# Performance work log

Measured on AMD Instinct MI355X. Metric: run time of the kernel, lower is better.

## Reference

```python
import jax, jax.numpy as jnp
import numpy as np

N = 100000       # nodes
E = 1600000      # edges per graph
D_IN, D_H, D_OUT = 256, 64, 32
TEM = (0.9, 0.8)  # tem[0], tem[1]


def setup_inputs() -> dict:
    key = jax.random.key(0)
    ks = jax.random.split(key, 17)
    f32 = jnp.float32
    return {
        "features": jax.random.normal(ks[0], (N, D_IN), f32),
        # GraphConv layer1: glorot-ish weight [in, out] + bias
        "W1": jax.random.normal(ks[1], (D_IN, D_H), f32) / np.sqrt(D_IN).astype(np.float32),
        "b1": jnp.zeros((D_H,), f32),
        "W2": jax.random.normal(ks[2], (D_H, D_OUT), f32) / np.sqrt(D_H).astype(np.float32),
        "b2": jnp.zeros((D_OUT,), f32),
        # gating linears: nn.Linear(2*d, 1) -> weight [1, 2*d], bias [1]
        "ga11_w": jax.random.normal(ks[3], (1, 2 * D_H), f32) * 0.1,
        "ga11_b": jnp.zeros((1,), f32),
        "ga12_w": jax.random.normal(ks[4], (1, 2 * D_H), f32) * 0.1,
        "ga12_b": jnp.zeros((1,), f32),
        "ga21_w": jax.random.normal(ks[5], (1, 2 * D_OUT), f32) * 0.1,
        "ga21_b": jnp.zeros((1,), f32),
        "ga22_w": jax.random.normal(ks[6], (1, 2 * D_OUT), f32) * 0.1,
        "ga22_b": jnp.zeros((1,), f32),
        # two graphs as edge lists over the same N nodes
        "src1": jax.random.randint(ks[7], (E,), 0, N, jnp.int32),
        "dst1": jax.random.randint(ks[8], (E,), 0, N, jnp.int32),
        "src2": jax.random.randint(ks[9], (E,), 0, N, jnp.int32),
        "dst2": jax.random.randint(ks[10], (E,), 0, N, jnp.int32),
    }


def _graph_conv(feat, W, b, src, dst):
    """DGL GraphConv, norm='both': D_dst^{-1/2} A^T D_src^{-1/2} X W + b.
    in_feats > out_feats for both layers, so W is applied before aggregation."""
    ones = jnp.ones(src.shape[0], feat.dtype)
    deg_out = jnp.clip(jax.ops.segment_sum(ones, src, num_segments=N), 1.0)  # [N]
    deg_in = jnp.clip(jax.ops.segment_sum(ones, dst, num_segments=N), 1.0)   # [N]
    h = (feat * jax.lax.rsqrt(deg_out)[:, None]) @ W                          # [N, d_out]
    agg = jax.ops.segment_sum(h[src], dst, num_segments=N)                    # SpMM scatter-add
    return agg * jax.lax.rsqrt(deg_in)[:, None] + b


def _gate(xa, xb, w, b, tem):
    """Faithful to: ga = softmax(Linear(cat[xa,xb]), dim=1); diag(ga) -> ga[0,0];
    xb' = tem * diag * xb. softmax over a size-1 axis gives ones; dropout is a
    no-op in eval mode."""
    ga = jnp.concatenate([xa, xb], axis=1) @ w.T + b  # [N, 1]
    ga = jax.nn.softmax(ga, axis=1)                   # all ones ([N,1], axis of size 1)
    d = ga[0, 0]                                      # torch.diag of [N,1] -> scalar ga[0,0]
    return tem * d * xb


def reference(features, W1, b1, W2, b2, ga11_w, ga11_b, ga12_w, ga12_b,
              ga21_w, ga21_b, ga22_w, ga22_b, src1, dst1, src2, dst2):
    x11 = _graph_conv(features, W1, b1, src1, dst1)
    x12 = _graph_conv(features, W1, b1, src2, dst2)
    x12 = _gate(x11, x12, ga11_w, ga11_b, TEM[1])
    x11 = _gate(x12, x11, ga12_w, ga12_b, TEM[0])
    x1 = x11 + x12
    x21 = _graph_conv(x1, W2, b2, src1, dst1)
    x22 = _graph_conv(x1, W2, b2, src2, dst2)
    x22 = _gate(x21, x22, ga21_w, ga21_b, TEM[1])
    x21 = _gate(x22, x21, ga22_w, ga22_b, TEM[0])
    return x21 + x22
```

## Files before the change

kernel.cpp:

```cpp
#include <hip/hip_runtime.h>
#include <hip/hip_bf16.h>

#define TEM0 0.9f
#define TEM1 0.8f
#define NPB 256
#define CAP 4608
#define CHUNKE 2048
#define MAXBUCK 512

typedef __attribute__((ext_vector_type(8))) short bf16x8;
typedef __attribute__((ext_vector_type(4))) float f32x4;

static __device__ __forceinline__ short f2bf(float x) {
  union { __hip_bfloat16 h; short s; } u;
  u.h = __float2bfloat16(x);
  return u.s;
}
static __device__ __forceinline__ float bf2f(short s) {
  union { float f; unsigned u; } v;
  v.u = ((unsigned)(unsigned short)s) << 16;
  return v.f;
}

__global__ __launch_bounds__(256) void bucket_gemm(
    const int* __restrict__ src1, const int* __restrict__ dst1,
    const int* __restrict__ src2, const int* __restrict__ dst2,
    int* gcur_d, int* gcur_s,
    int* __restrict__ rawD1, int* __restrict__ rawD2,
    unsigned char* __restrict__ rawS1, unsigned char* __restrict__ rawS2,
    int E, int NCH, int NBUCK,
    const float* __restrict__ X, const short* __restrict__ Wb,
    short* __restrict__ Yb, int n)
{
  __shared__ int outR[CHUNKE];
  __shared__ unsigned char outS[CHUNKE];
  __shared__ unsigned short tickD[CHUNKE];
  __shared__ unsigned short tickS[CHUNKE];
  __shared__ short bktD[CHUNKE];
  __shared__ short bktS[CHUNKE];
  __shared__ int histD[MAXBUCK], histS[MAXBUCK];
  __shared__ int strtD[MAXBUCK], strtS[MAXBUCK];
  __shared__ int baszD[MAXBUCK], baszS[MAXBUCK];
  __shared__ int wsumD[4], wsumS[4];

  const int nbB = 2 * NCH;
  const int nbG = (n + 63) / 64;
  const int half = nbB < nbG ? nbB : nbG;
  int bi = (int)blockIdx.x;
  bool isB;
  int bid;
  if (bi < 2 * half) { isB = ((bi & 1) == 0); bid = bi >> 1; }
  else               { isB = (nbB > nbG);     bid = bi - half; }

  if (isB) {
    int g = 0, cb = bid;
    if (cb >= NCH) { g = 1; cb -= NCH; }
    const int* src = g ? src2 : src1;
    const int* dst = g ? dst2 : dst1;
    int* rawD = g ? rawD2 : rawD1;
    unsigned char* rawS = g ? rawS2 : rawS1;
    int* curD = gcur_d + g * NBUCK;
    int* curS = gcur_s + g * NBUCK;
    int tid = threadIdx.x;
    int lane = tid & 63, wave = tid >> 6;
    int e0 = cb * CHUNKE;
    int K = min(CHUNKE, E - e0);

    histD[tid] = 0; histD[tid + 256] = 0;
    histS[tid] = 0; histS[tid + 256] = 0;
    __syncthreads();

    for (int i = tid; i < K; i += 256) {
      int d = dst[e0 + i], s = src[e0 + i];
      tickD[i] = (unsigned short)atomicAdd(&histD[d >> 8], 1);
      tickS[i] = (unsigned short)atomicAdd(&histS[s >> 8], 1);
    }
    __syncthreads();

    {
      int d0 = histD[2 * tid], d1 = histD[2 * tid + 1];
      int s0 = histS[2 * tid], s1 = histS[2 * tid + 1];
      int dv = d0 + d1, sv = s0 + s1;
      int vd = dv, vs = sv;
#pragma unroll
      for (int off = 1; off < 64; off <<= 1) {
        int td = __shfl_up(vd, off);
        int ts = __shfl_up(vs, off);
        if (lane >= off) { vd += td; vs += ts; }
      }
      if (lane == 63) { wsumD[wave] = vd; wsumS[wave] = vs; }
      __syncthreads();
      int wpD = 0, wpS = 0;
#pragma unroll
      for (int w0 = 0; w0 < 4; ++w0) {
        wpD += (w0 < wave) ? wsumD[w0] : 0;
        wpS += (w0 < wave) ? wsumS[w0] : 0;
      }
      int exD = wpD + vd - dv;
      int exS = wpS + vs - sv;
      strtD[2 * tid] = exD; strtD[2 * tid + 1] = exD + d0;
      strtS[2 * tid] = exS; strtS[2 * tid + 1] = exS + s0;
      for (int b = tid; b < NBUCK; b += 256) {
        int c = histD[b];
        baszD[b] = c ? atomicAdd(&curD[b], c) : 0;
        c = histS[b];
        baszS[b] = c ? atomicAdd(&curS[b], c) : 0;
      }
    }
    __syncthreads();

    for (int i = tid; i < K; i += 256) {
      int d = dst[e0 + i], s = src[e0 + i];
      int bD = d >> 8, bS = s >> 8;
      int qD = strtD[bD] + (int)tickD[i];
      int qS = strtS[bS] + (int)tickS[i];
      outR[qD] = ((d & 255) << 17) | s;
      bktD[qD] = (short)bD;
      outS[qS] = (unsigned char)(s & 255);
      bktS[qS] = (short)bS;
    }
    __syncthreads();

    for (int i = tid; i < K; i += 256) {
      int b = bktD[i];
      int off = baszD[b] + (i - strtD[b]);
      if (off < CAP) rawD[(size_t)b * CAP + off] = outR[i];
    }
    for (int i = tid; i < K; i += 256) {
      int b = bktS[i];
      int off = baszS[b] + (i - strtS[b]);
      if (off < CAP) rawS[(size_t)b * CAP + off] = outS[i];
    }
  } else {
    int w = threadIdx.x >> 6;
    int l = threadIdx.x & 63;
    int row = bid * 64 + w * 16 + (l & 15);
    int rowc = row < n ? row : n - 1;
    int ko = (l >> 4) << 3;

    f32x4 acc[4] = {};
    const float* xrow = X + (size_t)rowc * 256;

#pragma unroll
    for (int kk = 0; kk < 8; ++kk) {
      const float4* p = reinterpret_cast<const float4*>(xrow + kk * 32 + ko);
      float4 a0 = p[0], a1 = p[1];
      bf16x8 af;
      af[0] = f2bf(a0.x); af[1] = f2bf(a0.y); af[2] = f2bf(a0.z); af[3] = f2bf(a0.w);
      af[4] = f2bf(a1.x); af[5] = f2bf(a1.y); af[6] = f2bf(a1.z); af[7] = f2bf(a1.w);
#pragma unroll
      for (int ct = 0; ct < 4; ++ct) {
        bf16x8 bfrag = *reinterpret_cast<const bf16x8*>(Wb + ((size_t)(ct * 8 + kk) * 64 + l) * 8);
        acc[ct] = __builtin_amdgcn_mfma_f32_16x16x32_bf16(af, bfrag, acc[ct], 0, 0, 0);
      }
    }

    int r0 = bid * 64 + w * 16 + ((l >> 4) << 2);
    int c0 = l & 15;
#pragma unroll
    for (int ct = 0; ct < 4; ++ct) {
#pragma unroll
      for (int i = 0; i < 4; ++i) {
        int r = r0 + i;
        if (r < n) Yb[(size_t)r * 64 + ct * 16 + c0] = f2bf(acc[ct][i]);
      }
    }
  }
}

__global__ __launch_bounds__(256) void histsort(
    const int* __restrict__ gcur_s, const int* __restrict__ gcur_d,
    const unsigned char* __restrict__ rawS1, const unsigned char* __restrict__ rawS2,
    const int* __restrict__ rawD1, const int* __restrict__ rawD2,
    int* __restrict__ co1, int* __restrict__ co2,
    int* __restrict__ edata1, int* __restrict__ edata2,
    int* __restrict__ ci1, int* __restrict__ ci2,
    int* __restrict__ ns1, int* __restrict__ ns2, int NBUCK, int N)
{
  __shared__ int hist[NPB], strt[NPB];
  __shared__ short tick[CAP];
  __shared__ int sl[CAP];
  __shared__ int wsum[4];

  int bi = (int)blockIdx.x;
  bool isHist = ((bi & 1) == 0);
  int bid = bi >> 1;
  int g = 0, b = bid;
  if (b >= NBUCK) { g = 1; b -= NBUCK; }
  int tid = threadIdx.x;

  if (isHist) {
    const unsigned char* raw = (g ? rawS2 : rawS1) + (size_t)b * CAP;
    int* co = g ? co2 : co1;
    int K = gcur_s[g * NBUCK + b]; if (K > CAP) K = CAP;
    hist[tid] = 0;
    __syncthreads();
    for (int j = tid; j < K; j += 256) atomicAdd(&hist[raw[j]], 1);
    __syncthreads();
    int node = b * NPB + tid;
    if (node < N) co[node] = hist[tid];
  } else {
    const int* raw = (g ? rawD2 : rawD1) + (size_t)b * CAP;
    int* edata = g ? edata2 : edata1;
    int* ci = g ? ci2 : ci1;
    int* ns = g ? ns2 : ns1;
    int K = gcur_d[g * NBUCK + b]; if (K > CAP) K = CAP;
    int lane = tid & 63, wave = tid >> 6;

    hist[tid] = 0;
    __syncthreads();
    for (int j = tid; j < K; j += 256)
      tick[j] = (short)atomicAdd(&hist[raw[j] >> 17], 1);
    __syncthreads();
    int h = hist[tid], v = h;
#pragma unroll
    for (int off = 1; off < 64; off <<= 1) {
      int t = __shfl_up(v, off);
      if (lane >= off) v += t;
    }
    if (lane == 63) wsum[wave] = v;
    __syncthreads();
    int wpre = 0;
#pragma unroll
    for (int w0 = 0; w0 < 4; ++w0) wpre += (w0 < wave) ? wsum[w0] : 0;
    strt[tid] = wpre + v - h;
    __syncthreads();
    for (int j = tid; j < K; j += 256) {
      int r = raw[j];
      sl[strt[r >> 17] + tick[j]] = r & 0x1FFFF;
    }
    __syncthreads();
    size_t gbase = (size_t)b * CAP;
    for (int j = tid; j < K; j += 256) edata[gbase + j] = sl[j];
    int node = b * NPB + tid;
    if (node < N) { ci[node] = hist[tid]; ns[node] = (int)gbase + strt[tid]; }
  }
}

__global__ __launch_bounds__(256) void prep_w(
    const float* __restrict__ W1, const float* __restrict__ W2,
    short* __restrict__ Wb, short* __restrict__ Wb2)
{
  int t = blockIdx.x * 256 + threadIdx.x;
  if (t < 2048) {
    int lane = t & 63;
    int kk = (t >> 6) & 7;
    int ct = t >> 9;
    int col = ct * 16 + (lane & 15);
    int k0 = kk * 32 + ((lane >> 4) << 3);
#pragma unroll
    for (int i = 0; i < 8; ++i)
      Wb[(size_t)t * 8 + i] = f2bf(W1[(size_t)(k0 + i) * 64 + col]);
  } else if (t < 3072) {
    int t2 = t - 2048;
    int lane = t2 & 63;
    int kk = (t2 >> 6) & 1;
    int ct = t2 >> 7;
    int col = ct * 16 + (lane & 15);
    int k0 = kk * 32 + ((lane >> 4) << 3);
#pragma unroll
    for (int i = 0; i < 8; ++i)
      Wb2[(size_t)t2 * 8 + i] = f2bf(W2[(size_t)(k0 + i) * 32 + col]);
  }
}

__global__ __launch_bounds__(256) void gemm2_mfma(
    const short* __restrict__ X, const short* __restrict__ Wb2,
    short* __restrict__ Y2b, int n)
{
  int w = threadIdx.x >> 6;
  int l = threadIdx.x & 63;
  int row = blockIdx.x * 64 + w * 16 + (l & 15);
  int rowc = row < n ? row : n - 1;
  int ko = (l >> 4) << 3;

  f32x4 acc[2] = {};
  const short* xrow = X + (size_t)rowc * 64;

#pragma unroll
  for (int kk = 0; kk < 2; ++kk) {
    bf16x8 af = *reinterpret_cast<const bf16x8*>(xrow + kk * 32 + ko);
#pragma unroll
    for (int ct = 0; ct < 2; ++ct) {
      bf16x8 bfrag = *reinterpret_cast<const bf16x8*>(Wb2 + ((size_t)(ct * 2 + kk) * 64 + l) * 8);
      acc[ct] = __builtin_amdgcn_mfma_f32_16x16x32_bf16(af, bfrag, acc[ct], 0, 0, 0);
    }
  }

  int r0 = blockIdx.x * 64 + w * 16 + ((l >> 4) << 2);
  int c0 = l & 15;
#pragma unroll
  for (int ct = 0; ct < 2; ++ct) {
#pragma unroll
    for (int i = 0; i < 4; ++i) {
      int r = r0 + i;
      if (r < n) Y2b[(size_t)r * 32 + ct * 16 + c0] = f2bf(acc[ct][i]);
    }
  }
}

template<int D, bool BF16OUT>
__global__ __launch_bounds__(256) void gather_nodes_bf(
    const int* __restrict__ ci1, const int* __restrict__ ns1,
    const int* __restrict__ edata1, const int* __restrict__ co1,
    const int* __restrict__ ci2, const int* __restrict__ ns2,
    const int* __restrict__ edata2, const int* __restrict__ co2,
    const short* __restrict__ Yb, const float* __restrict__ bias,
    float bscale, float* __restrict__ outf, short* __restrict__ outb, int n)
{
  constexpr int LPR = D / 8;
  constexpr int EPI = 64 / LPR;
  int wid  = (blockIdx.x * 256 + threadIdx.x) >> 6;
  int lane = threadIdx.x & 63;
  int grp = lane / LPR;
  int li  = lane % LPR;
  if (wid >= n) return;

  const bf16x8* Y8 = reinterpret_cast<const bf16x8*>(Yb);
  float a1[8], a2[8];
#pragma unroll
  for (int k = 0; k < 8; ++k) { a1[k] = 0.f; a2[k] = 0.f; }

  int len1 = ci1[wid], st1 = ns1[wid];
  int len2 = ci2[wid], st2 = ns2[wid];
  int lmax = len1 > len2 ? len1 : len2;

#pragma unroll 2
  for (int j = grp; j < lmax; j += EPI) {
    bool p1 = j < len1, p2 = j < len2;
    int s1 = p1 ? edata1[st1 + j] : 0;
    int s2 = p2 ? edata2[st2 + j] : 0;
    float c1 = p1 ? TEM0 * rsqrtf((float)co1[s1]) : 0.f;
    float c2 = p2 ? TEM1 * rsqrtf((float)co2[s2]) : 0.f;
    bf16x8 v1 = Y8[(size_t)s1 * LPR + li];
    bf16x8 v2 = Y8[(size_t)s2 * LPR + li];
#pragma unroll
    for (int k = 0; k < 8; ++k) {
      a1[k] = fmaf(c1, bf2f(v1[k]), a1[k]);
      a2[k] = fmaf(c2, bf2f(v2[k]), a2[k]);
    }
  }

  float r1 = rsqrtf((float)(len1 < 1 ? 1 : len1));
  float r2 = rsqrtf((float)(len2 < 1 ? 1 : len2));
  float acc[8];
#pragma unroll
  for (int k = 0; k < 8; ++k) acc[k] = fmaf(r1, a1[k], r2 * a2[k]);

#pragma unroll
  for (int m = LPR; m < 64; m <<= 1) {
#pragma unroll
    for (int k = 0; k < 8; ++k) acc[k] += __shfl_xor(acc[k], m);
  }

  if (grp == 0) {
    float4 b0 = reinterpret_cast<const float4*>(bias)[li * 2];
    float4 b1v = reinterpret_cast<const float4*>(bias)[li * 2 + 1];
    float o[8];
    o[0] = fmaf(bscale, b0.x, acc[0]);
    o[1] = fmaf(bscale, b0.y, acc[1]);
    o[2] = fmaf(bscale, b0.z, acc[2]);
    o[3] = fmaf(bscale, b0.w, acc[3]);
    o[4] = fmaf(bscale, b1v.x, acc[4]);
    o[5] = fmaf(bscale, b1v.y, acc[5]);
    o[6] = fmaf(bscale, b1v.z, acc[6]);
    o[7] = fmaf(bscale, b1v.w, acc[7]);
    if constexpr (BF16OUT) {
      bf16x8 ov;
#pragma unroll
      for (int k = 0; k < 8; ++k) ov[k] = f2bf(o[k]);
      *reinterpret_cast<bf16x8*>(outb + (size_t)wid * D + li * 8) = ov;
    } else {
      float4 o0 = make_float4(o[0], o[1], o[2], o[3]);
      float4 o1 = make_float4(o[4], o[5], o[6], o[7]);
      float4* op = reinterpret_cast<float4*>(outf + (size_t)wid * D + li * 8);
      op[0] = o0;
      op[1] = o1;
    }
  }
}

extern "C" void kernel_launch(void* const* d_in, const int* in_sizes, int n_in,
                              void* d_out, int out_size, void* d_ws, size_t ws_size,
                              hipStream_t stream)
{
  const float* features = (const float*)d_in[0];
  const float* W1 = (const float*)d_in[1];
  const float* b1 = (const float*)d_in[2];
  const float* W2 = (const float*)d_in[3];
  const float* b2 = (const float*)d_in[4];
  const int* src1 = (const int*)d_in[13];
  const int* dst1 = (const int*)d_in[14];
  const int* src2 = (const int*)d_in[15];
  const int* dst2 = (const int*)d_in[16];

  const int N = in_sizes[0] / 256;
  const int E = in_sizes[13];
  const int NBUCK = (N + NPB - 1) / NPB;
  const int NCH = (E + CHUNKE - 1) / CHUNKE;

  char* ws = (char*)d_ws;
  int* gcur_d = (int*)ws;
  int* gcur_s = gcur_d + 2 * NBUCK;
  int* rawD1  = gcur_s + 2 * NBUCK;
  int* rawD2  = rawD1 + (size_t)NBUCK * CAP;
  unsigned char* rawS1 = (unsigned char*)(rawD2 + (size_t)NBUCK * CAP);
  unsigned char* rawS2 = rawS1 + (size_t)NBUCK * CAP;
  int* edata1 = (int*)(rawS2 + (size_t)NBUCK * CAP);
  int* edata2 = edata1 + (size_t)NBUCK * CAP;
  int* ci1 = edata2 + (size_t)NBUCK * CAP;
  int* ci2 = ci1 + N;
  int* ns1 = ci2 + N;
  int* ns2 = ns1 + N;
  int* co1 = ns2 + N;
  int* co2 = co1 + N;
  short* Yb  = (short*)(co2 + N);
  short* Y2b = Yb + (size_t)N * 64;
  short* x1b = Y2b + (size_t)N * 32;
  short* Wb  = x1b + (size_t)N * 64;
  short* Wb2 = Wb + 16384;
  float* out = (float*)d_out;

  (void)hipMemsetAsync(gcur_d, 0, (size_t)4 * NBUCK * sizeof(int), stream);
  prep_w<<<12, 256, 0, stream>>>(W1, W2, Wb, Wb2);

  const int nbGemm = (N + 63) / 64;
  bucket_gemm<<<2 * NCH + nbGemm, 256, 0, stream>>>(
      src1, dst1, src2, dst2, gcur_d, gcur_s,
      rawD1, rawD2, rawS1, rawS2, E, NCH, NBUCK,
      features, Wb, Yb, N);

  histsort<<<4 * NBUCK, 256, 0, stream>>>(
      gcur_s, gcur_d, rawS1, rawS2, rawD1, rawD2,
      co1, co2, edata1, edata2, ci1, ci2, ns1, ns2, NBUCK, N);

  gather_nodes_bf<64, true><<<(N + 3) / 4, 256, 0, stream>>>(
      ci1, ns1, edata1, co1, ci2, ns2, edata2, co2,
      Yb, b1, TEM0 + TEM1, nullptr, x1b, N);

  gemm2_mfma<<<nbGemm, 256, 0, stream>>>(x1b, Wb2, Y2b, N);

  gather_nodes_bf<32, false><<<(N + 3) / 4, 256, 0, stream>>>(
      ci1, ns1, edata1, co1, ci2, ns2, edata2, co2,
      Y2b, b2, TEM0 + TEM1, out, nullptr, N);
}
```

Before: 317.4 us.

## Pack per-edge source norm coefficient into edge index word, split histsort kernel

```diff
diff --git a/kernel.cpp b/kernel.cpp
--- a/kernel.cpp
+++ b/kernel.cpp
@@ -168,12 +168,31 @@
   }
 }
 
-__global__ __launch_bounds__(256) void histsort(
-    const int* __restrict__ gcur_s, const int* __restrict__ gcur_d,
+__global__ __launch_bounds__(256) void hist_src(
+    const int* __restrict__ gcur_s,
     const unsigned char* __restrict__ rawS1, const unsigned char* __restrict__ rawS2,
+    int* __restrict__ co1, int* __restrict__ co2, int NBUCK, int N)
+{
+  __shared__ int hist[NPB];
+  int g = 0, b = blockIdx.x;
+  if (b >= NBUCK) { g = 1; b -= NBUCK; }
+  const unsigned char* raw = (g ? rawS2 : rawS1) + (size_t)b * CAP;
+  int* co = g ? co2 : co1;
+  int K = gcur_s[g * NBUCK + b]; if (K > CAP) K = CAP;
+  int tid = threadIdx.x;
+  hist[tid] = 0;
+  __syncthreads();
+  for (int j = tid; j < K; j += 256) atomicAdd(&hist[raw[j]], 1);
+  __syncthreads();
+  int node = b * NPB + tid;
+  if (node < N) co[node] = hist[tid];
+}
+
+__global__ __launch_bounds__(256) void sort_dst(
+    const int* __restrict__ gcur_d,
     const int* __restrict__ rawD1, const int* __restrict__ rawD2,
-    int* __restrict__ co1, int* __restrict__ co2,
-    int* __restrict__ edata1, int* __restrict__ edata2,
+    unsigned* __restrict__ edata1, unsigned* __restrict__ edata2,
+    const int* __restrict__ co1, const int* __restrict__ co2,
     int* __restrict__ ci1, int* __restrict__ ci2,
     int* __restrict__ ns1, int* __restrict__ ns2, int NBUCK, int N)
 {
@@ -181,60 +200,50 @@
   __shared__ short tick[CAP];
   __shared__ int sl[CAP];
   __shared__ int wsum[4];
-
-  int bi = (int)blockIdx.x;
-  bool isHist = ((bi & 1) == 0);
-  int bid = bi >> 1;
-  int g = 0, b = bid;
+  int g = 0, b = blockIdx.x;
   if (b >= NBUCK) { g = 1; b -= NBUCK; }
+  const int* raw = (g ? rawD2 : rawD1) + (size_t)b * CAP;
+  unsigned* edata = g ? edata2 : edata1;
+  const int* co = g ? co2 : co1;
+  const float tem = g ? TEM1 : TEM0;
+  int* ci = g ? ci2 : ci1;
+  int* ns = g ? ns2 : ns1;
+  int K = gcur_d[g * NBUCK + b]; if (K > CAP) K = CAP;
   int tid = threadIdx.x;
-
-  if (isHist) {
-    const unsigned char* raw = (g ? rawS2 : rawS1) + (size_t)b * CAP;
-    int* co = g ? co2 : co1;
-    int K = gcur_s[g * NBUCK + b]; if (K > CAP) K = CAP;
-    hist[tid] = 0;
-    __syncthreads();
-    for (int j = tid; j < K; j += 256) atomicAdd(&hist[raw[j]], 1);
-    __syncthreads();
-    int node = b * NPB + tid;
-    if (node < N) co[node] = hist[tid];
-  } else {
-    const int* raw = (g ? rawD2 : rawD1) + (size_t)b * CAP;
-    int* edata = g ? edata2 : edata1;
-    int* ci = g ? ci2 : ci1;
-    int* ns = g ? ns2 : ns1;
-    int K = gcur_d[g * NBUCK + b]; if (K > CAP) K = CAP;
-    int lane = tid & 63, wave = tid >> 6;
-
-    hist[tid] = 0;
-    __syncthreads();
-    for (int j = tid; j < K; j += 256)
-      tick[j] = (short)atomicAdd(&hist[raw[j] >> 17], 1);
-    __syncthreads();
-    int h = hist[tid], v = h;
-#pragma unroll
-    for (int off = 1; off < 64; off <<= 1) {
-      int t = __shfl_up(v, off);
-      if (lane >= off) v += t;
-    }
-    if (lane == 63) wsum[wave] = v;
-    __syncthreads();
-    int wpre = 0;
-#pragma unroll
-    for (int w0 = 0; w0 < 4; ++w0) wpre += (w0 < wave) ? wsum[w0] : 0;
-    strt[tid] = wpre + v - h;
-    __syncthreads();
-    for (int j = tid; j < K; j += 256) {
-      int r = raw[j];
-      sl[strt[r >> 17] + tick[j]] = r & 0x1FFFF;
-    }
-    __syncthreads();
-    size_t gbase = (size_t)b * CAP;
-    for (int j = tid; j < K; j += 256) edata[gbase + j] = sl[j];
-    int node = b * NPB + tid;
-    if (node < N) { ci[node] = hist[tid]; ns[node] = (int)gbase + strt[tid]; }
-  }
+  int lane = tid & 63, wave = tid >> 6;
+
+  hist[tid] = 0;
+  __syncthreads();
+  for (int j = tid; j < K; j += 256)
+    tick[j] = (short)atomicAdd(&hist[raw[j] >> 17], 1);
+  __syncthreads();
+  int h = hist[tid], v = h;
+#pragma unroll
+  for (int off = 1; off < 64; off <<= 1) {
+    int t = __shfl_up(v, off);
+    if (lane >= off) v += t;
+  }
+  if (lane == 63) wsum[wave] = v;
+  __syncthreads();
+  int wpre = 0;
+#pragma unroll
+  for (int w0 = 0; w0 < 4; ++w0) wpre += (w0 < wave) ? wsum[w0] : 0;
+  strt[tid] = wpre + v - h;
+  __syncthreads();
+  for (int j = tid; j < K; j += 256) {
+    int r = raw[j];
+    sl[strt[r >> 17] + tick[j]] = r & 0x1FFFF;
+  }
+  __syncthreads();
+  size_t gbase = (size_t)b * CAP;
+  for (int j = tid; j < K; j += 256) {
+    int s = sl[j];
+    float c = tem * rsqrtf((float)co[s]);
+    unsigned cb = (unsigned)(unsigned short)f2bf(c) & 0x7FFFu;
+    edata[gbase + j] = (cb << 17) | (unsigned)s;
+  }
+  int node = b * NPB + tid;
+  if (node < N) { ci[node] = hist[tid]; ns[node] = (int)gbase + strt[tid]; }
 }
 
 __global__ __launch_bounds__(256) void prep_w(
@@ -251,7 +260,7 @@
 #pragma unroll
     for (int i = 0; i < 8; ++i)
       Wb[(size_t)t * 8 + i] = f2bf(W1[(size_t)(k0 + i) * 64 + col]);
-  } else if (t < 3072) {
+  } else if (t < 2048 + 256) {
     int t2 = t - 2048;
     int lane = t2 & 63;
     int kk = (t2 >> 6) & 1;
@@ -301,10 +310,8 @@
 
 template<int D, bool BF16OUT>
 __global__ __launch_bounds__(256) void gather_nodes_bf(
-    const int* __restrict__ ci1, const int* __restrict__ ns1,
-    const int* __restrict__ edata1, const int* __restrict__ co1,
-    const int* __restrict__ ci2, const int* __restrict__ ns2,
-    const int* __restrict__ edata2, const int* __restrict__ co2,
+    const int* __restrict__ ci1, const int* __restrict__ ns1, const unsigned* __restrict__ edata1,
+    const int* __restrict__ ci2, const int* __restrict__ ns2, const unsigned* __restrict__ edata2,
     const short* __restrict__ Yb, const float* __restrict__ bias,
     float bscale, float* __restrict__ outf, short* __restrict__ outb, int n)
 {
@@ -328,10 +335,12 @@
 #pragma unroll 2
   for (int j = grp; j < lmax; j += EPI) {
     bool p1 = j < len1, p2 = j < len2;
-    int s1 = p1 ? edata1[st1 + j] : 0;
-    int s2 = p2 ? edata2[st2 + j] : 0;
-    float c1 = p1 ? TEM0 * rsqrtf((float)co1[s1]) : 0.f;
-    float c2 = p2 ? TEM1 * rsqrtf((float)co2[s2]) : 0.f;
+    unsigned u1 = p1 ? edata1[st1 + j] : 0u;
+    unsigned u2 = p2 ? edata2[st2 + j] : 0u;
+    float c1 = __uint_as_float((u1 >> 17) << 16);
+    float c2 = __uint_as_float((u2 >> 17) << 16);
+    int s1 = (int)(u1 & 0x1FFFFu);
+    int s2 = (int)(u2 & 0x1FFFFu);
     bf16x8 v1 = Y8[(size_t)s1 * LPR + li];
     bf16x8 v2 = Y8[(size_t)s2 * LPR + li];
 #pragma unroll
@@ -406,9 +415,9 @@
   int* rawD2  = rawD1 + (size_t)NBUCK * CAP;
   unsigned char* rawS1 = (unsigned char*)(rawD2 + (size_t)NBUCK * CAP);
   unsigned char* rawS2 = rawS1 + (size_t)NBUCK * CAP;
-  int* edata1 = (int*)(rawS2 + (size_t)NBUCK * CAP);
-  int* edata2 = edata1 + (size_t)NBUCK * CAP;
-  int* ci1 = edata2 + (size_t)NBUCK * CAP;
+  unsigned* edata1 = (unsigned*)(rawS2 + (size_t)NBUCK * CAP);
+  unsigned* edata2 = edata1 + (size_t)NBUCK * CAP;
+  int* ci1 = (int*)(edata2 + (size_t)NBUCK * CAP);
   int* ci2 = ci1 + N;
   int* ns1 = ci2 + N;
   int* ns2 = ns1 + N;
@@ -422,7 +431,7 @@
   float* out = (float*)d_out;
 
   (void)hipMemsetAsync(gcur_d, 0, (size_t)4 * NBUCK * sizeof(int), stream);
-  prep_w<<<12, 256, 0, stream>>>(W1, W2, Wb, Wb2);
+  prep_w<<<9, 256, 0, stream>>>(W1, W2, Wb, Wb2);
 
   const int nbGemm = (N + 63) / 64;
   bucket_gemm<<<2 * NCH + nbGemm, 256, 0, stream>>>(
@@ -430,17 +439,15 @@
       rawD1, rawD2, rawS1, rawS2, E, NCH, NBUCK,
       features, Wb, Yb, N);
 
-  histsort<<<4 * NBUCK, 256, 0, stream>>>(
-      gcur_s, gcur_d, rawS1, rawS2, rawD1, rawD2,
-      co1, co2, edata1, edata2, ci1, ci2, ns1, ns2, NBUCK, N);
+  hist_src<<<2 * NBUCK, 256, 0, stream>>>(gcur_s, rawS1, rawS2, co1, co2, NBUCK, N);
+  sort_dst<<<2 * NBUCK, 256, 0, stream>>>(gcur_d, rawD1, rawD2, edata1, edata2,
+                                          co1, co2, ci1, ci2, ns1, ns2, NBUCK, N);
 
   gather_nodes_bf<64, true><<<(N + 3) / 4, 256, 0, stream>>>(
-      ci1, ns1, edata1, co1, ci2, ns2, edata2, co2,
-      Yb, b1, TEM0 + TEM1, nullptr, x1b, N);
+      ci1, ns1, edata1, ci2, ns2, edata2, Yb, b1, TEM0 + TEM1, nullptr, x1b, N);
 
   gemm2_mfma<<<nbGemm, 256, 0, stream>>>(x1b, Wb2, Y2b, N);
 
   gather_nodes_bf<32, false><<<(N + 3) / 4, 256, 0, stream>>>(
-      ci1, ns1, edata1, co1, ci2, ns2, edata2, co2,
-      Y2b, b2, TEM0 + TEM1, out, nullptr, N);
-}
+      ci1, ns1, edata1, ci2, ns2, edata2, Y2b, b2, TEM0 + TEM1, out, nullptr, N);
+}
```

Measured after the change: 275.9 us. 13.0% less time.
